# Kernel optimization log

Measured on AMD Instinct MI355X. Metric: run time of the kernel, lower is better.

## Reference

```python
import jax, jax.numpy as jnp
import numpy as np

N_NODES = 50000
N_EDGES = 800000
D_IN = 256
D_HID = 256
D_OUT = 8


def _glorot(key, shape):
    fan_in = shape[-1]
    bound = 1.0 / np.sqrt(fan_in)
    return jax.random.uniform(key, shape, minval=-bound, maxval=bound, dtype=jnp.float32)


def setup_inputs() -> dict:
    key = jax.random.key(0)
    ks = jax.random.split(key, 12)
    x = jax.random.normal(ks[0], (N_NODES, D_IN), dtype=jnp.float32)
    edge_index = jax.random.randint(ks[1], (2, N_EDGES), 0, N_NODES, dtype=jnp.int64)
    return {
        "x": x,
        "edge_index": edge_index,
        # SAGEConv1: lin_l (neighbor path, has bias), lin_r (root path, no bias)
        "W1l": _glorot(ks[2], (D_HID, D_IN)),
        "b1": jnp.zeros((D_HID,), jnp.float32),
        "W1r": _glorot(ks[3], (D_HID, D_IN)),
        # SAGEConv2
        "W2l": _glorot(ks[4], (D_HID, D_HID)),
        "b2": jnp.zeros((D_HID,), jnp.float32),
        "W2r": _glorot(ks[5], (D_HID, D_HID)),
        # MLP decoder
        "Wm1": _glorot(ks[6], (D_HID, D_HID)),
        "bm1": _glorot(ks[7], (D_HID,)),
        "Wm2": _glorot(ks[8], (D_OUT, D_HID)),
        "bm2": _glorot(ks[9], (D_OUT,)),
    }


def _sage_conv(x, edge_index, Wl, b, Wr):
    # PyG SAGEConv with mean aggregation:
    # out = lin_l(mean_{j in N(i)} x_j) + lin_r(x_i)
    src, dst = edge_index[0], edge_index[1]
    msg = x[src]  # [E, d] gather
    agg = jax.ops.segment_sum(msg, dst, num_segments=x.shape[0])  # [N, d]
    cnt = jax.ops.segment_sum(jnp.ones((edge_index.shape[1],), x.dtype), dst,
                              num_segments=x.shape[0])  # in-degree [N]
    mean = agg / jnp.maximum(cnt, 1.0)[:, None]
    return mean @ Wl.T + b + x @ Wr.T


def reference(x, edge_index, W1l, b1, W1r, W2l, b2, W2r, Wm1, bm1, Wm2, bm2):
    h = jax.nn.relu(_sage_conv(x, edge_index, W1l, b1, W1r))
    h = jax.nn.relu(_sage_conv(h, edge_index, W2l, b2, W2r))
    h = jax.nn.relu(h @ Wm1.T + bm1)
    logits = h @ Wm2.T + bm2
    return jax.nn.softmax(logits, axis=-1)
```

## Files before the change

### kernel.cpp

```cpp
#include <hip/hip_runtime.h>
#include <hip/hip_bf16.h>
#include <cstdint>
#include <cstddef>

#define D 256

typedef __attribute__((ext_vector_type(8))) short bf16x8;
typedef __attribute__((ext_vector_type(4))) float f32x4;
typedef __attribute__((ext_vector_type(4))) unsigned short ushort4v;
typedef __attribute__((ext_vector_type(8))) unsigned short ushort8v;

__device__ __forceinline__ unsigned short f2bf(float f) {
  union { float f; unsigned int u; } v; v.f = f;
  unsigned int u = v.u;
  u += ((u >> 16) & 1u) + 0x7fffu;
  return (unsigned short)(u >> 16);
}
__device__ __forceinline__ float bf2f(unsigned short s) {
  union { unsigned int u; float f; } v; v.u = ((unsigned int)s) << 16;
  return v.f;
}

#define GLL16(g, l) __builtin_amdgcn_global_load_lds( \
    (const __attribute__((address_space(1))) void*)(g), \
    (__attribute__((address_space(3))) void*)(l), 16, 0, 0)


__global__ __launch_bounds__(256) void k_deg(const int* __restrict__ dst,
                                             int* __restrict__ deg, int E) {
  int e = blockIdx.x * 256 + threadIdx.x;
  if (e < E) atomicAdd(&deg[dst[e]], 1);
}

__global__ __launch_bounds__(256) void k_bsum(const int* __restrict__ deg,
                                              int* __restrict__ bsum, int M) {
  __shared__ int sm[256];
  int tid = threadIdx.x;
  int base = blockIdx.x * 1024 + tid * 4;
  int s = 0;
#pragma unroll
  for (int i = 0; i < 4; ++i) s += (base + i < M) ? deg[base + i] : 0;
  sm[tid] = s;
  __syncthreads();
  for (int off = 128; off > 0; off >>= 1) {
    if (tid < off) sm[tid] += sm[tid + off];
    __syncthreads();
  }
  if (tid == 0) bsum[blockIdx.x] = sm[0];
}

__global__ __launch_bounds__(64) void k_scanb(const int* __restrict__ bsum,
                                              int* __restrict__ boff,
                                              int* __restrict__ row_ptr,
                                              int nb, int M) {
  int l = threadIdx.x;
  int orig = (l < nb) ? bsum[l] : 0;
  int v = orig;
  for (int off = 1; off < 64; off <<= 1) {
    int t = __shfl_up(v, off);
    if (l >= off) v += t;
  }
  if (l < nb) boff[l] = v - orig;
  if (l == nb - 1) row_ptr[M] = v;
}

__global__ __launch_bounds__(256) void k_apply(const int* __restrict__ deg,
                                               const int* __restrict__ boff,
                                               int* __restrict__ row_ptr,
                                               int* __restrict__ cursor, int M) {
  __shared__ int sm[256];
  int tid = threadIdx.x;
  int base = blockIdx.x * 1024 + tid * 4;
  int d[4], p[4];
#pragma unroll
  for (int i = 0; i < 4; ++i) d[i] = (base + i < M) ? deg[base + i] : 0;
  p[0] = 0; p[1] = d[0]; p[2] = d[0] + d[1]; p[3] = d[0] + d[1] + d[2];
  int s = p[3] + d[3];
  sm[tid] = s;
  __syncthreads();
  for (int off = 1; off < 256; off <<= 1) {
    int t = (tid >= off) ? sm[tid - off] : 0;
    __syncthreads();
    sm[tid] += t;
    __syncthreads();
  }
  int excl = sm[tid] - s + boff[blockIdx.x];
#pragma unroll
  for (int i = 0; i < 4; ++i) {
    if (base + i < M) {
      row_ptr[base + i] = excl + p[i];
      cursor[base + i] = excl + p[i];
    }
  }
}

__global__ __launch_bounds__(256) void k_fill(const int* __restrict__ src,
                                              const int* __restrict__ dst,
                                              int* __restrict__ cursor,
                                              int* __restrict__ col, int E) {
  int e = blockIdx.x * 256 + threadIdx.x;
  if (e < E) {
    int p = atomicAdd(&cursor[dst[e]], 1);
    col[p] = src[e];
  }
}


__global__ __launch_bounds__(256) void k_split(const float* __restrict__ in,
                                               unsigned short* __restrict__ oh,
                                               unsigned short* __restrict__ ol,
                                               int n4) {
  int i = blockIdx.x * 256 + threadIdx.x;
  if (i >= n4) return;
  float4 v = ((const float4*)in)[i];
  float a[4] = {v.x, v.y, v.z, v.w};
  ushort4v h, l;
#pragma unroll
  for (int j = 0; j < 4; ++j) {
    h[j] = f2bf(a[j]);
    l[j] = f2bf(a[j] - bf2f(h[j]));
  }
  ((ushort4v*)oh)[i] = h;
  ((ushort4v*)ol)[i] = l;
}

__global__ __launch_bounds__(256) void k_splitw(
    const float* __restrict__ s0, const float* __restrict__ s1,
    const float* __restrict__ s2, const float* __restrict__ s3,
    const float* __restrict__ s4,
    unsigned short* __restrict__ h0, unsigned short* __restrict__ l0,
    unsigned short* __restrict__ h1, unsigned short* __restrict__ l1,
    unsigned short* __restrict__ h2, unsigned short* __restrict__ l2,
    unsigned short* __restrict__ h3, unsigned short* __restrict__ l3,
    unsigned short* __restrict__ h4, unsigned short* __restrict__ l4) {
  const float* s; unsigned short* oh; unsigned short* ol;
  switch (blockIdx.y) {
    case 0: s = s0; oh = h0; ol = l0; break;
    case 1: s = s1; oh = h1; ol = l1; break;
    case 2: s = s2; oh = h2; ol = l2; break;
    case 3: s = s3; oh = h3; ol = l3; break;
    default: s = s4; oh = h4; ol = l4; break;
  }
  int i = blockIdx.x * 256 + threadIdx.x;
  float4 v = ((const float4*)s)[i];
  float a[4] = {v.x, v.y, v.z, v.w};
  ushort4v h, l;
#pragma unroll
  for (int j = 0; j < 4; ++j) {
    h[j] = f2bf(a[j]);
    l[j] = f2bf(a[j] - bf2f(h[j]));
  }
  ((ushort4v*)oh)[i] = h;
  ((ushort4v*)ol)[i] = l;
}


__global__ __launch_bounds__(256) void k_gemm_mfma(
    const unsigned short* __restrict__ Ah, const unsigned short* __restrict__ Al,
    const unsigned short* __restrict__ Wh, const unsigned short* __restrict__ Wl,
    unsigned short* __restrict__ outBF, float* __restrict__ outF32,
    const float* __restrict__ bias, int M, int NBF, int NF, int relu,
    int nbxshift) {
  __shared__ char lds[65536];

  const int tid = threadIdx.x;
  const int wave = tid >> 6;
  const int lane = tid & 63;

  int nwg = gridDim.x;
  int id = blockIdx.x;
  int q = nwg >> 3, r = nwg & 7;
  int xcd = id & 7, j = id >> 3;
  int w = ((xcd < r) ? xcd * (q + 1) : r * (q + 1) + (xcd - r) * q) + j;
  const int by = w >> nbxshift;
  const int bx = w & ((1 << nbxshift) - 1);
  const int n0 = bx * 128;

  int aoff[2], woff[2], ldso[2];
#pragma unroll
  for (int rr = 0; rr < 2; ++rr) {
    int o = rr * 4096 + wave * 1024 + lane * 16;
    int row = o >> 6;
    int sp = (o >> 4) & 3;
    int sl = sp ^ ((row >> 1) & 3);
    int arow = by * 128 + row; if (arow > M - 1) arow = M - 1;
    aoff[rr] = arow * 256 + sl * 8;
    woff[rr] = (n0 + row) * 256 + sl * 8;
    ldso[rr] = rr * 4096 + wave * 1024;
  }

  const int rbase = (wave >> 1) * 64;
  const int cbase = (wave & 1) * 64;
  const int fr = lane & 15;
  const int g = lane >> 4;

  int a_addr[4], w_addr[4];
#pragma unroll
  for (int m = 0; m < 4; ++m) {
    int row = rbase + m * 16 + fr;
    a_addr[m] = row * 64 + ((g ^ ((row >> 1) & 3)) * 16);
  }
#pragma unroll
  for (int n = 0; n < 4; ++n) {
    int row = cbase + n * 16 + fr;
    w_addr[n] = row * 64 + ((g ^ ((row >> 1) & 3)) * 16);
  }

  f32x4 acc[4][4] = {};

#pragma unroll
  for (int rr = 0; rr < 2; ++rr) {
    GLL16(Ah + aoff[rr], lds + 0     + ldso[rr]);
    GLL16(Al + aoff[rr], lds + 8192  + ldso[rr]);
    GLL16(Wh + woff[rr], lds + 16384 + ldso[rr]);
    GLL16(Wl + woff[rr], lds + 24576 + ldso[rr]);
  }

  for (int t = 0; t < 8; ++t) {
    const int cb = (t & 1) * 32768;
    if (t < 7) {
      const int nb = ((t + 1) & 1) * 32768;
      const int ko = (t + 1) * 32;
#pragma unroll
      for (int rr = 0; rr < 2; ++rr) {
        GLL16(Ah + aoff[rr] + ko, lds + nb + 0     + ldso[rr]);
        GLL16(Al + aoff[rr] + ko, lds + nb + 8192  + ldso[rr]);
        GLL16(Wh + woff[rr] + ko, lds + nb + 16384 + ldso[rr]);
        GLL16(Wl + woff[rr] + ko, lds + nb + 24576 + ldso[rr]);
      }
      asm volatile("s_waitcnt vmcnt(8)" ::: "memory");
    } else {
      asm volatile("s_waitcnt vmcnt(0)" ::: "memory");
    }
    __builtin_amdgcn_s_barrier();

    bf16x8 ah[4], al[4], wh[4], wl[4];
#pragma unroll
    for (int m = 0; m < 4; ++m) {
      ah[m] = *(const bf16x8*)(lds + cb + 0    + a_addr[m]);
      al[m] = *(const bf16x8*)(lds + cb + 8192 + a_addr[m]);
    }
#pragma unroll
    for (int n = 0; n < 4; ++n) {
      wh[n] = *(const bf16x8*)(lds + cb + 16384 + w_addr[n]);
      wl[n] = *(const bf16x8*)(lds + cb + 24576 + w_addr[n]);
    }
#pragma unroll
    for (int m = 0; m < 4; ++m)
#pragma unroll
      for (int n = 0; n < 4; ++n) {
        acc[m][n] = __builtin_amdgcn_mfma_f32_16x16x32_bf16(ah[m], wh[n], acc[m][n], 0, 0, 0);
        acc[m][n] = __builtin_amdgcn_mfma_f32_16x16x32_bf16(ah[m], wl[n], acc[m][n], 0, 0, 0);
        acc[m][n] = __builtin_amdgcn_mfma_f32_16x16x32_bf16(al[m], wh[n], acc[m][n], 0, 0, 0);
      }
    __builtin_amdgcn_s_barrier();
  }

#pragma unroll
  for (int n = 0; n < 4; ++n) {
    int col = n0 + cbase + n * 16 + fr;
    bool isbf = col < NBF;
    int fcol = col - NBF;
    float bv = (!isbf && bias) ? bias[fcol] : 0.f;
#pragma unroll
    for (int m = 0; m < 4; ++m) {
      f32x4 a = acc[m][n];
#pragma unroll
      for (int rr = 0; rr < 4; ++rr) {
        int row = by * 128 + rbase + m * 16 + g * 4 + rr;
        if (row < M) {
          if (isbf) {
            outBF[(size_t)row * NBF + col] = f2bf(a[rr]);
          } else {
            float v = a[rr] + bv;
            if (relu) v = fmaxf(v, 0.f);
            outF32[(size_t)row * NF + fcol] = v;
          }
        }
      }
    }
  }
}


__global__ __launch_bounds__(256) void k_agg2(const unsigned short* __restrict__ T1,
                                              const float* __restrict__ T2,
                                              unsigned short* __restrict__ Hh,
                                              unsigned short* __restrict__ Hl,
                                              const int* __restrict__ row_ptr,
                                              const int* __restrict__ col, int M) {
  int wave = threadIdx.x >> 6, lane = threadIdx.x & 63;
  int n = blockIdx.x * 4 + wave;
  if (n >= M) return;
  int beg = row_ptr[n], end = row_ptr[n + 1];
  int half = lane >> 5, sl = lane & 31;
  float s[8] = {0.f, 0.f, 0.f, 0.f, 0.f, 0.f, 0.f, 0.f};
  int j = beg + half;
  for (; j + 2 < end; j += 4) {
    int i0 = col[j];
    int i1 = col[j + 2];
    ushort8v v0 = *(const ushort8v*)(T1 + (size_t)i0 * 256 + sl * 8);
    ushort8v v1 = *(const ushort8v*)(T1 + (size_t)i1 * 256 + sl * 8);
#pragma unroll
    for (int i = 0; i < 8; ++i) s[i] += bf2f(v0[i]) + bf2f(v1[i]);
  }
  for (; j < end; j += 2) {
    int i0 = col[j];
    ushort8v v0 = *(const ushort8v*)(T1 + (size_t)i0 * 256 + sl * 8);
#pragma unroll
    for (int i = 0; i < 8; ++i) s[i] += bf2f(v0[i]);
  }
#pragma unroll
  for (int i = 0; i < 8; ++i) s[i] += __shfl_xor(s[i], 32);
  int dg = end - beg;
  float inv = 1.0f / (float)(dg > 0 ? dg : 1);
  const float4* t2p = (const float4*)(T2 + (size_t)n * 256 + sl * 8);
  float4 ta = t2p[0], tb = t2p[1];
  float h[8];
  h[0] = fmaxf(s[0] * inv + ta.x, 0.f);
  h[1] = fmaxf(s[1] * inv + ta.y, 0.f);
  h[2] = fmaxf(s[2] * inv + ta.z, 0.f);
  h[3] = fmaxf(s[3] * inv + ta.w, 0.f);
  h[4] = fmaxf(s[4] * inv + tb.x, 0.f);
  h[5] = fmaxf(s[5] * inv + tb.y, 0.f);
  h[6] = fmaxf(s[6] * inv + tb.z, 0.f);
  h[7] = fmaxf(s[7] * inv + tb.w, 0.f);
  if (half == 0) {
    ushort8v hh;
#pragma unroll
    for (int i = 0; i < 8; ++i) hh[i] = f2bf(h[i]);
    *(ushort8v*)(Hh + (size_t)n * 256 + sl * 8) = hh;
  } else {
    ushort8v hl;
#pragma unroll
    for (int i = 0; i < 8; ++i) {
      unsigned short hi = f2bf(h[i]);
      hl[i] = f2bf(h[i] - bf2f(hi));
    }
    *(ushort8v*)(Hl + (size_t)n * 256 + sl * 8) = hl;
  }
}


__global__ __launch_bounds__(256) void k_final(const float* __restrict__ H,
                                               const float* __restrict__ Wm2,
                                               const float* __restrict__ bm2,
                                               float* __restrict__ out, int M) {
  int node = blockIdx.x * 4 + (threadIdx.x >> 6);
  int lane = threadIdx.x & 63;
  if (node >= M) return;
  int o = lane >> 3;
  int r = lane & 7;
  const float* h = H + (size_t)node * D;
  const float* w = Wm2 + (size_t)o * D;
  float p = 0.f;
  for (int k = r; k < D; k += 8) p += h[k] * w[k];
  p += __shfl_xor(p, 1);
  p += __shfl_xor(p, 2);
  p += __shfl_xor(p, 4);
  float logit = p + bm2[o];
  float m = logit;
  m = fmaxf(m, __shfl_xor(m, 8));
  m = fmaxf(m, __shfl_xor(m, 16));
  m = fmaxf(m, __shfl_xor(m, 32));
  float e = expf(logit - m);
  float s = e;
  s += __shfl_xor(s, 8);
  s += __shfl_xor(s, 16);
  s += __shfl_xor(s, 32);
  if (r == 0) out[(size_t)node * 8 + o] = e / s;
}


extern "C" void kernel_launch(void* const* d_in, const int* in_sizes, int n_in,
                              void* d_out, int out_size, void* d_ws, size_t ws_size,
                              hipStream_t stream) {
  const float* x   = (const float*)d_in[0];
  const int*   ei  = (const int*)d_in[1];
  const float* W1l = (const float*)d_in[2];
  const float* b1  = (const float*)d_in[3];
  const float* W1r = (const float*)d_in[4];
  const float* W2l = (const float*)d_in[5];
  const float* b2  = (const float*)d_in[6];
  const float* W2r = (const float*)d_in[7];
  const float* Wm1 = (const float*)d_in[8];
  const float* bm1 = (const float*)d_in[9];
  const float* Wm2 = (const float*)d_in[10];
  const float* bm2 = (const float*)d_in[11];
  float* out = (float*)d_out;

  int M = in_sizes[0] / D;
  int E = in_sizes[1] / 2;
  const int* src = ei;
  const int* dst = ei + E;

  char* p = (char*)d_ws;
  auto alloc = [&](size_t bytes) {
    char* q = p;
    p += (bytes + 255) & ~(size_t)255;
    return q;
  };
  unsigned short* bh0  = (unsigned short*)alloc((size_t)M * 256 * 2);
  unsigned short* bh1  = (unsigned short*)alloc((size_t)M * 256 * 2);
  unsigned short* T1bf = (unsigned short*)alloc((size_t)M * 256 * 2);
  float*          T2f  = (float*)alloc((size_t)M * 256 * 4);
  unsigned short* Wc1h = (unsigned short*)alloc(512 * 256 * 2);
  unsigned short* Wc1l = (unsigned short*)alloc(512 * 256 * 2);
  unsigned short* Wc2h = (unsigned short*)alloc(512 * 256 * 2);
  unsigned short* Wc2l = (unsigned short*)alloc(512 * 256 * 2);
  unsigned short* Wm1h = (unsigned short*)alloc(256 * 256 * 2);
  unsigned short* Wm1l = (unsigned short*)alloc(256 * 256 * 2);
  int* deg     = (int*)alloc((size_t)M * 4);
  int* row_ptr = (int*)alloc((size_t)(M + 1) * 4);
  int* cursor  = (int*)alloc((size_t)M * 4);
  int* col     = (int*)alloc((size_t)E * 4);
  int* bsum    = (int*)alloc(64 * 4);
  int* boff    = (int*)alloc(64 * 4);

  int nb = (M + 1023) / 1024;

  hipMemsetAsync(deg, 0, (size_t)M * sizeof(int), stream);
  k_deg<<<dim3((E + 255) / 256), dim3(256), 0, stream>>>(dst, deg, E);
  k_bsum<<<dim3(nb), dim3(256), 0, stream>>>(deg, bsum, M);
  k_scanb<<<dim3(1), dim3(64), 0, stream>>>(bsum, boff, row_ptr, nb, M);
  k_apply<<<dim3(nb), dim3(256), 0, stream>>>(deg, boff, row_ptr, cursor, M);
  k_fill<<<dim3((E + 255) / 256), dim3(256), 0, stream>>>(src, dst, cursor, col, E);

  int nx4 = M * 256 / 4;
  k_split<<<dim3((nx4 + 255) / 256), dim3(256), 0, stream>>>(x, bh0, bh1, nx4);
  k_splitw<<<dim3(64, 5), dim3(256), 0, stream>>>(
      W1l, W1r, W2l, W2r, Wm1,
      Wc1h, Wc1l, Wc1h + 65536, Wc1l + 65536,
      Wc2h, Wc2l, Wc2h + 65536, Wc2l + 65536,
      Wm1h, Wm1l);

  dim3 blk(256);
  int nwg4 = ((M + 127) / 128) * 4;
  int nwg2 = ((M + 127) / 128) * 2;
  int aggGrid = (M + 3) / 4;

  k_gemm_mfma<<<dim3(nwg4), blk, 0, stream>>>(bh0, bh1, Wc1h, Wc1l, T1bf, T2f, b1, M, 256, 256, 0, 2);
  k_agg2<<<dim3(aggGrid), blk, 0, stream>>>(T1bf, T2f, bh0, bh1, row_ptr, col, M);
  k_gemm_mfma<<<dim3(nwg4), blk, 0, stream>>>(bh0, bh1, Wc2h, Wc2l, T1bf, T2f, b2, M, 256, 256, 0, 2);
  k_agg2<<<dim3(aggGrid), blk, 0, stream>>>(T1bf, T2f, bh0, bh1, row_ptr, col, M);
  k_gemm_mfma<<<dim3(nwg2), blk, 0, stream>>>(bh0, bh1, Wm1h, Wm1l, nullptr, T2f, bm1, M, 0, 256, 1, 1);
  k_final<<<dim3((M + 3) / 4), blk, 0, stream>>>(T2f, Wm2, bm2, out, M);
}
```

Before: 571.0 us.

## Make GEMM persistent with cross-tile prefetch, widen aggregation gather, use bf16 MLP hidden

The GEMM kernel becomes persistent: it launches 512 workgroups, each looping over its XCD's tile chunk and prefetching the next tile's first K-slice during the last iteration of the current one. The aggregation kernel now has each quarter-wave gather whole 512-byte rows, with 16 lanes covering a row, and reduces across quarters with shuffles. The MLP hidden layer is written as bf16 with bias and relu fused, and the final kernel reads bf16 with vectorised loads. Together these cut launch and tail overhead and memory traffic, at the cost of more register pressure and bf16 rounding of the decoder hidden state.

```diff
diff --git a/kernel.cpp b/kernel.cpp
--- a/kernel.cpp
+++ b/kernel.cpp
@@ -159,33 +159,29 @@
     const unsigned short* __restrict__ Ah, const unsigned short* __restrict__ Al,
     const unsigned short* __restrict__ Wh, const unsigned short* __restrict__ Wl,
     unsigned short* __restrict__ outBF, float* __restrict__ outF32,
-    const float* __restrict__ bias, int M, int NBF, int NF, int relu,
-    int nbxshift) {
+    const float* __restrict__ biasF, const float* __restrict__ biasB,
+    int M, int NBF, int NF, int relu, int nbxshift, int NT) {
   __shared__ char lds[65536];
 
   const int tid = threadIdx.x;
   const int wave = tid >> 6;
   const int lane = tid & 63;
 
-  int nwg = gridDim.x;
-  int id = blockIdx.x;
-  int q = nwg >> 3, r = nwg & 7;
-  int xcd = id & 7, j = id >> 3;
-  int w = ((xcd < r) ? xcd * (q + 1) : r * (q + 1) + (xcd - r) * q) + j;
-  const int by = w >> nbxshift;
-  const int bx = w & ((1 << nbxshift) - 1);
-  const int n0 = bx * 128;
-
-  int aoff[2], woff[2], ldso[2];
+  const int xcd = blockIdx.x & 7;
+  const int ib = blockIdx.x >> 3;
+  const int q = NT >> 3, r = NT & 7;
+  const int csz = q + (xcd < r ? 1 : 0);
+  const int cb0 = (xcd < r) ? xcd * (q + 1) : r * (q + 1) + (xcd - r) * q;
+  if (ib >= csz) return;
+  const int bxmask = (1 << nbxshift) - 1;
+
+  int ldso[2], srow[2], sslot[2];
 #pragma unroll
   for (int rr = 0; rr < 2; ++rr) {
     int o = rr * 4096 + wave * 1024 + lane * 16;
-    int row = o >> 6;
+    srow[rr] = o >> 6;
     int sp = (o >> 4) & 3;
-    int sl = sp ^ ((row >> 1) & 3);
-    int arow = by * 128 + row; if (arow > M - 1) arow = M - 1;
-    aoff[rr] = arow * 256 + sl * 8;
-    woff[rr] = (n0 + row) * 256 + sl * 8;
+    sslot[rr] = sp ^ ((srow[rr] >> 1) & 3);
     ldso[rr] = rr * 4096 + wave * 1024;
   }
 
@@ -206,8 +202,20 @@
     w_addr[n] = row * 64 + ((g ^ ((row >> 1) & 3)) * 16);
   }
 
-  f32x4 acc[4][4] = {};
-
+  auto mkoffs = [&](int w, int* ao, int* wo) {
+    int by = w >> nbxshift;
+    int n0 = (w & bxmask) * 128;
+#pragma unroll
+    for (int rr = 0; rr < 2; ++rr) {
+      int arow = by * 128 + srow[rr];
+      if (arow > M - 1) arow = M - 1;
+      ao[rr] = arow * 256 + sslot[rr] * 8;
+      wo[rr] = (n0 + srow[rr]) * 256 + sslot[rr] * 8;
+    }
+  };
+
+  int aoff[2], woff[2];
+  mkoffs(cb0 + ib, aoff, woff);
 #pragma unroll
   for (int rr = 0; rr < 2; ++rr) {
     GLL16(Ah + aoff[rr], lds + 0     + ldso[rr]);
@@ -216,65 +224,104 @@
     GLL16(Wl + woff[rr], lds + 24576 + ldso[rr]);
   }
 
-  for (int t = 0; t < 8; ++t) {
-    const int cb = (t & 1) * 32768;
-    if (t < 7) {
-      const int nb = ((t + 1) & 1) * 32768;
-      const int ko = (t + 1) * 32;
-#pragma unroll
-      for (int rr = 0; rr < 2; ++rr) {
-        GLL16(Ah + aoff[rr] + ko, lds + nb + 0     + ldso[rr]);
-        GLL16(Al + aoff[rr] + ko, lds + nb + 8192  + ldso[rr]);
-        GLL16(Wh + woff[rr] + ko, lds + nb + 16384 + ldso[rr]);
-        GLL16(Wl + woff[rr] + ko, lds + nb + 24576 + ldso[rr]);
+  for (int j = ib; j < csz; j += 64) {
+    const int w = cb0 + j;
+    const int by = w >> nbxshift;
+    const int n0 = (w & bxmask) * 128;
+    mkoffs(w, aoff, woff);
+    const int hasnext = (j + 64 < csz);
+    int naoff[2], nwoff[2];
+    if (hasnext) mkoffs(w - (w & bxmask) ? 0 : 0, naoff, nwoff);
+    if (hasnext) mkoffs(cb0 + j + 64, naoff, nwoff);
+
+    f32x4 acc[4][4] = {};
+
+#pragma unroll
+    for (int t = 0; t < 8; ++t) {
+      const int cb = (t & 1) * 32768;
+      if (t < 7) {
+        const int nbuf = ((t + 1) & 1) * 32768;
+        const int ko = (t + 1) * 32;
+#pragma unroll
+        for (int rr = 0; rr < 2; ++rr) {
+          GLL16(Ah + aoff[rr] + ko, lds + nbuf + 0     + ldso[rr]);
+          GLL16(Al + aoff[rr] + ko, lds + nbuf + 8192  + ldso[rr]);
+          GLL16(Wh + woff[rr] + ko, lds + nbuf + 16384 + ldso[rr]);
+          GLL16(Wl + woff[rr] + ko, lds + nbuf + 24576 + ldso[rr]);
+        }
+        asm volatile("s_waitcnt vmcnt(8)" ::: "memory");
+      } else if (hasnext) {
+#pragma unroll
+        for (int rr = 0; rr < 2; ++rr) {
+          GLL16(Ah + naoff[rr], lds + 0     + ldso[rr]);
+          GLL16(Al + naoff[rr], lds + 8192  + ldso[rr]);
+          GLL16(Wh + nwoff[rr], lds + 16384 + ldso[rr]);
+          GLL16(Wl + nwoff[rr], lds + 24576 + ldso[rr]);
+        }
+        asm volatile("s_waitcnt vmcnt(8)" ::: "memory");
+      } else {
+        asm volatile("s_waitcnt vmcnt(0)" ::: "memory");
       }
-      asm volatile("s_waitcnt vmcnt(8)" ::: "memory");
+      __builtin_amdgcn_s_barrier();
+
+      bf16x8 ah[4], al[4], wh[4], wl[4];
+#pragma unroll
+      for (int m = 0; m < 4; ++m) {
+        ah[m] = *(const bf16x8*)(lds + cb + 0    + a_addr[m]);
+        al[m] = *(const bf16x8*)(lds + cb + 8192 + a_addr[m]);
+      }
+#pragma unroll
+      for (int n = 0; n < 4; ++n) {
+        wh[n] = *(const bf16x8*)(lds + cb + 16384 + w_addr[n]);
+        wl[n] = *(const bf16x8*)(lds + cb + 24576 + w_addr[n]);
+      }
+#pragma unroll
+      for (int m = 0; m < 4; ++m)
+#pragma unroll
+        for (int n = 0; n < 4; ++n) {
+          acc[m][n] = __builtin_amdgcn_mfma_f32_16x16x32_bf16(ah[m], wh[n], acc[m][n], 0, 0, 0);
+          acc[m][n] = __builtin_amdgcn_mfma_f32_16x16x32_bf16(ah[m], wl[n], acc[m][n], 0, 0, 0);
+          acc[m][n] = __builtin_amdgcn_mfma_f32_16x16x32_bf16(al[m], wh[n], acc[m][n], 0, 0, 0);
+        }
+      __builtin_amdgcn_s_barrier();
+    }
+
+    if (n0 < NBF) {
+#pragma unroll
+      for (int n = 0; n < 4; ++n) {
+        int col = n0 + cbase + n * 16 + fr;
+        float bvb = biasB ? biasB[col] : 0.f;
+#pragma unroll
+        for (int m = 0; m < 4; ++m) {
+          f32x4 a = acc[m][n];
+#pragma unroll
+          for (int rr = 0; rr < 4; ++rr) {
+            int row = by * 128 + rbase + m * 16 + g * 4 + rr;
+            if (row < M) {
+              float v = a[rr] + bvb;
+              if (biasB) v = fmaxf(v, 0.f);
+              outBF[(size_t)row * NBF + col] = f2bf(v);
+            }
+          }
+        }
+      }
     } else {
-      asm volatile("s_waitcnt vmcnt(0)" ::: "memory");
-    }
-    __builtin_amdgcn_s_barrier();
-
-    bf16x8 ah[4], al[4], wh[4], wl[4];
-#pragma unroll
-    for (int m = 0; m < 4; ++m) {
-      ah[m] = *(const bf16x8*)(lds + cb + 0    + a_addr[m]);
-      al[m] = *(const bf16x8*)(lds + cb + 8192 + a_addr[m]);
-    }
-#pragma unroll
-    for (int n = 0; n < 4; ++n) {
-      wh[n] = *(const bf16x8*)(lds + cb + 16384 + w_addr[n]);
-      wl[n] = *(const bf16x8*)(lds + cb + 24576 + w_addr[n]);
-    }
-#pragma unroll
-    for (int m = 0; m < 4; ++m)
 #pragma unroll
       for (int n = 0; n < 4; ++n) {
-        acc[m][n] = __builtin_amdgcn_mfma_f32_16x16x32_bf16(ah[m], wh[n], acc[m][n], 0, 0, 0);
-        acc[m][n] = __builtin_amdgcn_mfma_f32_16x16x32_bf16(ah[m], wl[n], acc[m][n], 0, 0, 0);
-        acc[m][n] = __builtin_amdgcn_mfma_f32_16x16x32_bf16(al[m], wh[n], acc[m][n], 0, 0, 0);
-      }
-    __builtin_amdgcn_s_barrier();
-  }
-
-#pragma unroll
-  for (int n = 0; n < 4; ++n) {
-    int col = n0 + cbase + n * 16 + fr;
-    bool isbf = col < NBF;
-    int fcol = col - NBF;
-    float bv = (!isbf && bias) ? bias[fcol] : 0.f;
-#pragma unroll
-    for (int m = 0; m < 4; ++m) {
-      f32x4 a = acc[m][n];
-#pragma unroll
-      for (int rr = 0; rr < 4; ++rr) {
-        int row = by * 128 + rbase + m * 16 + g * 4 + rr;
-        if (row < M) {
-          if (isbf) {
-            outBF[(size_t)row * NBF + col] = f2bf(a[rr]);
-          } else {
-            float v = a[rr] + bv;
-            if (relu) v = fmaxf(v, 0.f);
-            outF32[(size_t)row * NF + fcol] = v;
+        int col = n0 + cbase + n * 16 + fr;
+        int fcol = col - NBF;
+        float bv = biasF ? biasF[fcol] : 0.f;
+#pragma unroll
+        for (int m = 0; m < 4; ++m) {
+          f32x4 a = acc[m][n];
+#pragma unroll
+          for (int rr = 0; rr < 4; ++rr) {
+            int row = by * 128 + rbase + m * 16 + g * 4 + rr;
+            if (row < M) {
+              float v = a[rr] + bv;
+              if (relu) v = fmaxf(v, 0.f);
+              outF32[(size_t)row * NF + fcol] = v;
+            }
           }
         }
       }
@@ -293,43 +340,48 @@
   int n = blockIdx.x * 4 + wave;
   if (n >= M) return;
   int beg = row_ptr[n], end = row_ptr[n + 1];
-  int half = lane >> 5, sl = lane & 31;
-  float s[8] = {0.f, 0.f, 0.f, 0.f, 0.f, 0.f, 0.f, 0.f};
-  int j = beg + half;
-  for (; j + 2 < end; j += 4) {
-    int i0 = col[j];
-    int i1 = col[j + 2];
-    ushort8v v0 = *(const ushort8v*)(T1 + (size_t)i0 * 256 + sl * 8);
-    ushort8v v1 = *(const ushort8v*)(T1 + (size_t)i1 * 256 + sl * 8);
-#pragma unroll
-    for (int i = 0; i < 8; ++i) s[i] += bf2f(v0[i]) + bf2f(v1[i]);
-  }
-  for (; j < end; j += 2) {
-    int i0 = col[j];
-    ushort8v v0 = *(const ushort8v*)(T1 + (size_t)i0 * 256 + sl * 8);
-#pragma unroll
-    for (int i = 0; i < 8; ++i) s[i] += bf2f(v0[i]);
-  }
-#pragma unroll
-  for (int i = 0; i < 8; ++i) s[i] += __shfl_xor(s[i], 32);
+  int qt = lane >> 4;
+  int ql = lane & 15;
+  float s[16];
+#pragma unroll
+  for (int i = 0; i < 16; ++i) s[i] = 0.f;
+  int j = beg;
+  for (; j + 4 <= end; j += 4) {
+    int e = col[j + qt];
+    const ushort8v* pr = (const ushort8v*)(T1 + (size_t)e * 256 + ql * 16);
+    ushort8v v0 = pr[0];
+    ushort8v v1 = pr[1];
+#pragma unroll
+    for (int i = 0; i < 8; ++i) { s[i] += bf2f(v0[i]); s[8 + i] += bf2f(v1[i]); }
+  }
+  if (j + qt < end) {
+    int e = col[j + qt];
+    const ushort8v* pr = (const ushort8v*)(T1 + (size_t)e * 256 + ql * 16);
+    ushort8v v0 = pr[0];
+    ushort8v v1 = pr[1];
+#pragma unroll
+    for (int i = 0; i < 8; ++i) { s[i] += bf2f(v0[i]); s[8 + i] += bf2f(v1[i]); }
+  }
+#pragma unroll
+  for (int i = 0; i < 16; ++i) {
+    s[i] += __shfl_xor(s[i], 16);
+    s[i] += __shfl_xor(s[i], 32);
+  }
   int dg = end - beg;
   float inv = 1.0f / (float)(dg > 0 ? dg : 1);
-  const float4* t2p = (const float4*)(T2 + (size_t)n * 256 + sl * 8);
+  int eb = ql * 16 + (qt & 1) * 8;
+  int sb = (qt & 1) * 8;
+  const float4* t2p = (const float4*)(T2 + (size_t)n * 256 + eb);
   float4 ta = t2p[0], tb = t2p[1];
+  float t2v[8] = {ta.x, ta.y, ta.z, ta.w, tb.x, tb.y, tb.z, tb.w};
   float h[8];
-  h[0] = fmaxf(s[0] * inv + ta.x, 0.f);
-  h[1] = fmaxf(s[1] * inv + ta.y, 0.f);
-  h[2] = fmaxf(s[2] * inv + ta.z, 0.f);
-  h[3] = fmaxf(s[3] * inv + ta.w, 0.f);
-  h[4] = fmaxf(s[4] * inv + tb.x, 0.f);
-  h[5] = fmaxf(s[5] * inv + tb.y, 0.f);
-  h[6] = fmaxf(s[6] * inv + tb.z, 0.f);
-  h[7] = fmaxf(s[7] * inv + tb.w, 0.f);
-  if (half == 0) {
+#pragma unroll
+  for (int i = 0; i < 8; ++i) h[i] = fmaxf(s[sb + i] * inv + t2v[i], 0.f);
+  if (qt < 2) {
     ushort8v hh;
 #pragma unroll
     for (int i = 0; i < 8; ++i) hh[i] = f2bf(h[i]);
-    *(ushort8v*)(Hh + (size_t)n * 256 + sl * 8) = hh;
+    *(ushort8v*)(Hh + (size_t)n * 256 + eb) = hh;
   } else {
     ushort8v hl;
 #pragma unroll
@@ -337,12 +389,12 @@
       unsigned short hi = f2bf(h[i]);
       hl[i] = f2bf(h[i] - bf2f(hi));
     }
-    *(ushort8v*)(Hl + (size_t)n * 256 + sl * 8) = hl;
-  }
-}
-
-
-__global__ __launch_bounds__(256) void k_final(const float* __restrict__ H,
+    *(ushort8v*)(Hl + (size_t)n * 256 + eb) = hl;
+  }
+}
+
+
+__global__ __launch_bounds__(256) void k_final(const unsigned short* __restrict__ H,
                                                const float* __restrict__ Wm2,
                                                const float* __restrict__ bm2,
                                                float* __restrict__ out, int M) {
@@ -351,10 +403,17 @@
   if (node >= M) return;
   int o = lane >> 3;
   int r = lane & 7;
-  const float* h = H + (size_t)node * D;
-  const float* w = Wm2 + (size_t)o * D;
+  const unsigned short* h = H + (size_t)node * D + r * 32;
+  const float* w = Wm2 + (size_t)o * D + r * 32;
   float p = 0.f;
-  for (int k = r; k < D; k += 8) p += h[k] * w[k];
+#pragma unroll
+  for (int c = 0; c < 4; ++c) {
+    ushort8v hv = ((const ushort8v*)h)[c];
+    float4 w0 = ((const float4*)w)[c * 2];
+    float4 w1 = ((const float4*)w)[c * 2 + 1];
+    p += bf2f(hv[0]) * w0.x + bf2f(hv[1]) * w0.y + bf2f(hv[2]) * w0.z + bf2f(hv[3]) * w0.w;
+    p += bf2f(hv[4]) * w1.x + bf2f(hv[5]) * w1.y + bf2f(hv[6]) * w1.z + bf2f(hv[7]) * w1.w;
+  }
   p += __shfl_xor(p, 1);
   p += __shfl_xor(p, 2);
   p += __shfl_xor(p, 4);
@@ -364,11 +423,11 @@
   m = fmaxf(m, __shfl_xor(m, 16));
   m = fmaxf(m, __shfl_xor(m, 32));
   float e = expf(logit - m);
-  float s = e;
-  s += __shfl_xor(s, 8);
-  s += __shfl_xor(s, 16);
-  s += __shfl_xor(s, 32);
-  if (r == 0) out[(size_t)node * 8 + o] = e / s;
+  float ssum = e;
+  ssum += __shfl_xor(ssum, 8);
+  ssum += __shfl_xor(ssum, 16);
+  ssum += __shfl_xor(ssum, 32);
+  if (r == 0) out[(size_t)node * 8 + o] = e / ssum;
 }
 
 
@@ -435,14 +494,17 @@
       Wm1h, Wm1l);
 
   dim3 blk(256);
-  int nwg4 = ((M + 127) / 128) * 4;
-  int nwg2 = ((M + 127) / 128) * 2;
+  int NT4 = ((M + 127) / 128) * 4;
+  int NT2 = ((M + 127) / 128) * 2;
   int aggGrid = (M + 3) / 4;
 
-  k_gemm_mfma<<<dim3(nwg4), blk, 0, stream>>>(bh0, bh1, Wc1h, Wc1l, T1bf, T2f, b1, M, 256, 256, 0, 2);
+  k_gemm_mfma<<<dim3(512), blk, 0, stream>>>(bh0, bh1, Wc1h, Wc1l, T1bf, T2f,
+                                             b1, nullptr, M, 256, 256, 0, 2, NT4);
   k_agg2<<<dim3(aggGrid), blk, 0, stream>>>(T1bf, T2f, bh0, bh1, row_ptr, col, M);
-  k_gemm_mfma<<<dim3(nwg4), blk, 0, stream>>>(bh0, bh1, Wc2h, Wc2l, T1bf, T2f, b2, M, 256, 256, 0, 2);
+  k_gemm_mfma<<<dim3(512), blk, 0, stream>>>(bh0, bh1, Wc2h, Wc2l, T1bf, T2f,
+                                             b2, nullptr, M, 256, 256, 0, 2, NT4);
   k_agg2<<<dim3(aggGrid), blk, 0, stream>>>(T1bf, T2f, bh0, bh1, row_ptr, col, M);
-  k_gemm_mfma<<<dim3(nwg2), blk, 0, stream>>>(bh0, bh1, Wm1h, Wm1l, nullptr, T2f, bm1, M, 0, 256, 1, 1);
-  k_final<<<dim3((M + 3) / 4), blk, 0, stream>>>(T2f, Wm2, bm2, out, M);
-}
+  k_gemm_mfma<<<dim3(512), blk, 0, stream>>>(bh0, bh1, Wm1h, Wm1l, T1bf, nullptr,
+                                             nullptr, bm1, M, 256, 0, 1, 1, NT2);
+  k_final<<<dim3((M + 3) / 4), blk, 0, stream>>>(T1bf, Wm2, bm2, out, M);
+}
```

Measured after the change: 584.2 us. 1.02x slower.
